# Kernel tuning notes

Hardware: AMD Instinct MI355X
Metric: run time of the kernel (lower is better)

Reference implementation:

```python
import jax, jax.numpy as jnp
import numpy as np

NUM_HEADS = 16
HEAD_DIM = 64
D_MODEL = NUM_HEADS * HEAD_DIM  # 1024
FEATURE_DIM = 2 * HEAD_DIM      # 128


def setup_inputs() -> dict:
    key = jax.random.key(0)
    ks = jax.random.split(key, 6)
    B, S = 4, 8192
    scale = D_MODEL ** -0.5
    x = jax.random.normal(ks[0], (B, S, D_MODEL), dtype=jnp.float32)
    Wq = jax.random.normal(ks[1], (D_MODEL, D_MODEL), dtype=jnp.float32) * scale
    Wk = jax.random.normal(ks[2], (D_MODEL, D_MODEL), dtype=jnp.float32) * scale
    Wv = jax.random.normal(ks[3], (D_MODEL, D_MODEL), dtype=jnp.float32) * scale
    Wo = jax.random.normal(ks[4], (D_MODEL, D_MODEL), dtype=jnp.float32) * scale
    # random_features buffer: [head_dim, feature_dim], scaled by head_dim**-0.5
    rf = jax.random.normal(ks[5], (HEAD_DIM, FEATURE_DIM), dtype=jnp.float32) * (HEAD_DIM ** -0.5)
    return {"x": x, "Wq": Wq, "Wk": Wk, "Wv": Wv, "Wo": Wo, "rf": rf}


def _phi(x, rf):
    # x: [B, H, S, head_dim] -> [B, H, S, feature_dim]
    proj = jnp.matmul(x, rf)  # [B, H, S, 2*head_dim]
    cos_p, sin_p = jnp.split(proj, 2, axis=-1)
    return jnp.concatenate([jnp.cos(cos_p), jnp.sin(sin_p)], axis=-1) * (FEATURE_DIM ** -0.5)


def reference(x, Wq, Wk, Wv, Wo, rf):
    B, S, _ = x.shape
    def heads(y):  # [B, S, D] -> [B, H, S, head_dim]
        return y.reshape(B, S, NUM_HEADS, HEAD_DIM).transpose(0, 2, 1, 3)
    Q = heads(x @ Wq)
    K = heads(x @ Wk)
    V = heads(x @ Wv)
    Qp = _phi(Q, rf)  # [B, H, S, F]
    Kp = _phi(K, rf)
    KV = jnp.einsum('bhsf,bhsd->bhfd', Kp, V)        # [B, H, F, head_dim]
    QKV = jnp.einsum('bhsf,bhfd->bhsd', Qp, KV)      # [B, H, S, head_dim]
    Z = jnp.einsum('bhsf,bhf->bhs', Qp, Kp.sum(axis=2))[..., None]
    Z = jnp.clip(Z, 1e-6, None)
    out = (QKV / Z).transpose(0, 2, 1, 3).reshape(B, S, D_MODEL)
    return out @ Wo
```

## Files before the change

### kernel.cpp

```cpp
#include <hip/hip_runtime.h>
#include <stdint.h>


#define DEVINL __device__ __forceinline__

typedef float f32x4 __attribute__((ext_vector_type(4)));
typedef __bf16 bf16x8 __attribute__((ext_vector_type(8)));
typedef unsigned short u16;

#define TSTR 136
#define RSTR 72

DEVINL u16 f2bf(float f) {
  union { float f; uint32_t u; } v; v.f = f;
  uint32_t u = v.u;
  u += 0x7fffu + ((u >> 16) & 1u);
  return (u16)(u >> 16);
}
DEVINL float bf2f(u16 h) {
  union { uint32_t u; float f; } v; v.u = ((uint32_t)h) << 16;
  return v.f;
}

#define GLOAD16(gp, lp) __builtin_amdgcn_global_load_lds( \
    (const __attribute__((address_space(1))) unsigned int*)(gp), \
    (__attribute__((address_space(3))) unsigned int*)(lp), 16, 0, 0)

template <int ROWS>
DEVINL void stage_r128(const uint8_t* g, size_t stride, u16* lds, int wave, int lane) {
#pragma unroll
  for (int j = 0; j < ROWS / 32; ++j) {
    int row = wave * (ROWS / 4) + j * 8 + (lane >> 3);
    GLOAD16(g + (size_t)row * stride + (size_t)(lane & 7) * 16,
            (uint8_t*)lds + (size_t)(wave * (ROWS / 4) + j * 8) * 128);
  }
}

template <int ROWS>
DEVINL void stage_r256(const uint8_t* g, size_t stride, u16* lds, int wave, int lane) {
#pragma unroll
  for (int j = 0; j < ROWS / 16; ++j) {
    int row = wave * (ROWS / 4) + j * 4 + (lane >> 4);
    GLOAD16(g + (size_t)row * stride + (size_t)(lane & 15) * 16,
            (uint8_t*)lds + (size_t)(wave * (ROWS / 4) + j * 4) * 256);
  }
}

DEVINL void stage128_sw(const uint8_t* g, size_t stride, u16* lds, int wave, int lane) {
  const int c = (lane & 7) ^ (lane >> 3);
#pragma unroll
  for (int j = 0; j < 4; ++j) {
    int row = wave * 32 + j * 8 + (lane >> 3);
    GLOAD16(g + (size_t)row * stride + (size_t)c * 16,
            (uint8_t*)lds + (size_t)(wave * 32 + j * 8) * 128);
  }
}

DEVINL void mma128_sw(const u16* As, const u16* Bs, f32x4 acc[4][4],
                      int wr, int wc, int lane) {
#pragma unroll
  for (int kk = 0; kk < 2; ++kk) {
    const int cw = kk * 4 + (lane >> 4);
    const int sw = (cw ^ (lane & 7)) * 8;
    bf16x8 a[4], b[4];
#pragma unroll
    for (int m = 0; m < 4; ++m)
      a[m] = *(const bf16x8*)&As[(size_t)(wr * 64 + m * 16 + (lane & 15)) * 64 + sw];
#pragma unroll
    for (int n = 0; n < 4; ++n)
      b[n] = *(const bf16x8*)&Bs[(size_t)(wc * 64 + n * 16 + (lane & 15)) * 64 + sw];
#pragma unroll
    for (int m = 0; m < 4; ++m)
#pragma unroll
      for (int n = 0; n < 4; ++n)
        acc[m][n] = __builtin_amdgcn_mfma_f32_16x16x32_bf16(a[m], b[n], acc[m][n], 0, 0, 0);
  }
}


__global__ __launch_bounds__(256) void cast_x_kernel(
    const float* __restrict__ src, u16* __restrict__ dst, long n4) {
  long i = (long)blockIdx.x * 256 + threadIdx.x;
  const long stride = (long)gridDim.x * 256;
  const float4* s4 = (const float4*)src;
  uint2* d4 = (uint2*)dst;
  for (; i < n4; i += stride) {
    float4 v = s4[i];
    uint2 o;
    o.x = (uint32_t)f2bf(v.x) | ((uint32_t)f2bf(v.y) << 16);
    o.y = (uint32_t)f2bf(v.z) | ((uint32_t)f2bf(v.w) << 16);
    d4[i] = o;
  }
}

__global__ __launch_bounds__(256) void transpose_cast_kernel(
    const float* __restrict__ src, u16* __restrict__ dst, int R, int C) {
  __shared__ float tile[32 * 33];
  const int ntr = R >> 5;
  const int tr = blockIdx.x % ntr, tc = blockIdx.x / ntr;
  const int tid = threadIdx.x;
  {
    int r = tid >> 3, c4 = (tid & 7) * 4;
    float4 v = *(const float4*)&src[(size_t)(tr * 32 + r) * C + tc * 32 + c4];
    tile[r * 33 + c4 + 0] = v.x;
    tile[r * 33 + c4 + 1] = v.y;
    tile[r * 33 + c4 + 2] = v.z;
    tile[r * 33 + c4 + 3] = v.w;
  }
  __syncthreads();
  {
    int c = tid >> 3, r4 = (tid & 7) * 4;
    uint2 o;
    o.x = (uint32_t)f2bf(tile[(r4 + 0) * 33 + c]) |
          ((uint32_t)f2bf(tile[(r4 + 1) * 33 + c]) << 16);
    o.y = (uint32_t)f2bf(tile[(r4 + 2) * 33 + c]) |
          ((uint32_t)f2bf(tile[(r4 + 3) * 33 + c]) << 16);
    *(uint2*)&dst[(size_t)(tc * 32 + c) * R + tr * 32 + r4] = o;
  }
}

__global__ __launch_bounds__(256, 3) void gemm_qkv_phi_kernel(
    const u16* __restrict__ xb, const u16* __restrict__ wT,
    const u16* __restrict__ rfT,
    u16* __restrict__ Qp, u16* __restrict__ KpT, u16* __restrict__ VhT) {
  __shared__ u16 smem[26624];
  u16* As = smem;
  u16* Bs = smem + 8192;
  u16* Rs = smem + 17408;
  const int tid = threadIdx.x, lane = tid & 63, wave = tid >> 6;
  const int wr = wave >> 1, wc = wave & 1;
  const int nb = (blockIdx.x & 7) * 768 + (blockIdx.x >> 3);
  const int tn = nb % 24, tm = nb / 24;
  const int tensor = tn >> 3;

  f32x4 acc[4][4];
#pragma unroll
  for (int m = 0; m < 4; ++m)
#pragma unroll
    for (int n = 0; n < 4; ++n) acc[m][n] = (f32x4){0.f, 0.f, 0.f, 0.f};

  const uint8_t* aB = (const uint8_t*)(xb + (size_t)tm * 128 * 1024);
  const uint8_t* bB = (const uint8_t*)(wT + (size_t)tn * 128 * 1024);
  for (int kt = 0; kt < 16; ++kt) {
    stage128_sw(aB + kt * 128, 2048, As, wave, lane);
    stage128_sw(bB + kt * 128, 2048, Bs, wave, lane);
    __syncthreads();
    mma128_sw(As, Bs, acc, wr, wc, lane);
    __syncthreads();
  }

  const int b = (tm * 128) >> 13;
  const int sblk = (tm * 128) & 8191;

  if (tensor == 2) {
#pragma unroll
    for (int m = 0; m < 4; ++m) {
      int sl = wr * 64 + m * 16 + (lane >> 4) * 4;
#pragma unroll
      for (int n = 0; n < 4; ++n) {
        int cl = wc * 64 + n * 16 + (lane & 15);
#pragma unroll
        for (int r = 0; r < 4; ++r) smem[cl * TSTR + sl + r] = f2bf(acc[m][n][r]);
      }
    }
    __syncthreads();
#pragma unroll
    for (int it = 0; it < 8; ++it) {
      int cl = it * 16 + (tid >> 4);
      int c = (tn & 7) * 128 + cl;
      int h = c >> 6, d = c & 63;
      size_t off = ((size_t)((b * 16 + h) * 64 + d)) * 8192 + sblk + (tid & 15) * 8;
      *(uint4*)&VhT[off] = *(const uint4*)&smem[cl * TSTR + (tid & 15) * 8];
    }
    return;
  }

#pragma unroll
  for (int m = 0; m < 4; ++m) {
    int sl = wr * 64 + m * 16 + (lane >> 4) * 4;
#pragma unroll
    for (int n = 0; n < 4; ++n) {
      int cl = wc * 64 + n * 16 + (lane & 15);
#pragma unroll
      for (int r = 0; r < 4; ++r) smem[(sl + r) * TSTR + cl] = f2bf(acc[m][n][r]);
    }
  }
#pragma unroll
  for (int p4 = 0; p4 < 4; ++p4) {
    int idx = p4 * 256 + tid;
    int f = idx >> 3, c = idx & 7;
    *(uint4*)&Rs[f * RSTR + c * 8] = *(const uint4*)&rfT[f * 64 + c * 8];
  }
  __syncthreads();

  bf16x8 afr[2][2][2];
#pragma unroll
  for (int hh = 0; hh < 2; ++hh)
#pragma unroll
    for (int kk = 0; kk < 2; ++kk) {
      const int ko = kk * 32 + (lane >> 4) * 8;
#pragma unroll
      for (int m = 0; m < 2; ++m)
        afr[hh][kk][m] = *(const bf16x8*)&smem[
            (size_t)(wave * 32 + m * 16 + (lane & 15)) * TSTR + hh * 64 + ko];
    }
  __syncthreads();

  const float SC = 0.088388347648318447f;
#pragma unroll
  for (int hh = 0; hh < 2; ++hh) {
    const int h = (tn & 7) * 2 + hh;
    f32x4 p[2][8];
#pragma unroll
    for (int m = 0; m < 2; ++m)
#pragma unroll
      for (int n = 0; n < 8; ++n) p[m][n] = (f32x4){0.f, 0.f, 0.f, 0.f};
#pragma unroll
    for (int kk = 0; kk < 2; ++kk) {
      const int ko = kk * 32 + (lane >> 4) * 8;
      bf16x8 bb[8];
#pragma unroll
      for (int n = 0; n < 8; ++n)
        bb[n] = *(const bf16x8*)&Rs[(size_t)(n * 16 + (lane & 15)) * RSTR + ko];
#pragma unroll
      for (int m = 0; m < 2; ++m)
#pragma unroll
        for (int n = 0; n < 8; ++n)
          p[m][n] = __builtin_amdgcn_mfma_f32_16x16x32_bf16(afr[hh][kk][m], bb[n], p[m][n], 0, 0, 0);
    }

    if (tensor == 0) {
#pragma unroll
      for (int m = 0; m < 2; ++m)
#pragma unroll
        for (int n = 0; n < 8; ++n) {
          int f = n * 16 + (lane & 15);
          int sl = wave * 32 + m * 16 + (lane >> 4) * 4;
#pragma unroll
          for (int r = 0; r < 4; ++r) {
            float v = ((n < 4) ? __cosf(p[m][n][r]) : __sinf(p[m][n][r])) * SC;
            smem[(sl + r) * TSTR + f] = f2bf(v);
          }
        }
      __syncthreads();
      const size_t base_bh = (size_t)(b * 16 + h) * 8192;
#pragma unroll
      for (int it = 0; it < 8; ++it) {
        int s = it * 16 + (tid >> 4);
        *(uint4*)&Qp[(base_bh + sblk + s) * 128 + (tid & 15) * 8] =
            *(const uint4*)&smem[s * TSTR + (tid & 15) * 8];
      }
    } else {
#pragma unroll
      for (int m = 0; m < 2; ++m)
#pragma unroll
        for (int n = 0; n < 8; ++n) {
          int f = n * 16 + (lane & 15);
          int sl = wave * 32 + m * 16 + (lane >> 4) * 4;
#pragma unroll
          for (int r = 0; r < 4; ++r) {
            float v = ((n < 4) ? __cosf(p[m][n][r]) : __sinf(p[m][n][r])) * SC;
            smem[f * TSTR + sl + r] = f2bf(v);
          }
        }
      __syncthreads();
#pragma unroll
      for (int it = 0; it < 8; ++it) {
        int f = it * 16 + (tid >> 4);
        *(uint4*)&KpT[((size_t)(b * 16 + h) * 128 + f) * 8192 + sblk + (tid & 15) * 8] =
            *(const uint4*)&smem[f * TSTR + (tid & 15) * 8];
      }
    }
    if (hh == 0) __syncthreads();
  }
}

__global__ __launch_bounds__(256) void kv_partial_kernel(
    const u16* __restrict__ KpT, const u16* __restrict__ VhT,
    float* __restrict__ partial) {
  __shared__ u16 smem[12288];
  __shared__ float ksmem[256];
  u16* As = smem;
  u16* Bs = smem + 8192;
  const int tid = threadIdx.x, lane = tid & 63, wave = tid >> 6;
  const int bh = blockIdx.x >> 3, ch = blockIdx.x & 7;
  const uint8_t* aB = (const uint8_t*)(KpT + (size_t)bh * 128 * 8192 + ch * 1024);
  const uint8_t* bB = (const uint8_t*)(VhT + (size_t)bh * 64 * 8192 + ch * 1024);

  f32x4 acc[2][4];
#pragma unroll
  for (int m = 0; m < 2; ++m)
#pragma unroll
    for (int n = 0; n < 4; ++n) acc[m][n] = (f32x4){0.f, 0.f, 0.f, 0.f};
  float ks = 0.f;
  const int fK = tid >> 1, sO = (tid & 1) * 32;

  for (int t = 0; t < 16; ++t) {
    stage_r128<128>(aB + t * 128, 16384, As, wave, lane);
    stage_r128<64>(bB + t * 128, 16384, Bs, wave, lane);
    __syncthreads();
#pragma unroll
    for (int i = 0; i < 4; ++i) {
      uint4 v = *(const uint4*)&As[fK * 64 + sO + i * 8];
      ks += bf2f((u16)(v.x & 0xffff)) + bf2f((u16)(v.x >> 16));
      ks += bf2f((u16)(v.y & 0xffff)) + bf2f((u16)(v.y >> 16));
      ks += bf2f((u16)(v.z & 0xffff)) + bf2f((u16)(v.z >> 16));
      ks += bf2f((u16)(v.w & 0xffff)) + bf2f((u16)(v.w >> 16));
    }
#pragma unroll
    for (int kk = 0; kk < 2; ++kk) {
      const int ko = kk * 32 + (lane >> 4) * 8;
      bf16x8 a[2], bb[4];
#pragma unroll
      for (int m = 0; m < 2; ++m)
        a[m] = *(const bf16x8*)&As[(size_t)(wave * 32 + m * 16 + (lane & 15)) * 64 + ko];
#pragma unroll
      for (int n = 0; n < 4; ++n)
        bb[n] = *(const bf16x8*)&Bs[(size_t)(n * 16 + (lane & 15)) * 64 + ko];
#pragma unroll
      for (int m = 0; m < 2; ++m)
#pragma unroll
        for (int n = 0; n < 4; ++n)
          acc[m][n] = __builtin_amdgcn_mfma_f32_16x16x32_bf16(a[m], bb[n], acc[m][n], 0, 0, 0);
    }
    __syncthreads();
  }

  float* pb = partial + (size_t)blockIdx.x * (128 * 65);
#pragma unroll
  for (int m = 0; m < 2; ++m)
#pragma unroll
    for (int n = 0; n < 4; ++n) {
      int d = n * 16 + (lane & 15);
#pragma unroll
      for (int r = 0; r < 4; ++r) {
        int f = wave * 32 + m * 16 + (lane >> 4) * 4 + r;
        pb[f * 65 + d] = acc[m][n][r];
      }
    }
  ksmem[tid] = ks;
  __syncthreads();
  if (tid < 128) pb[tid * 65 + 64] = ksmem[2 * tid] + ksmem[2 * tid + 1];
}

__global__ __launch_bounds__(256) void kv_reduce_kernel(
    const float* __restrict__ partial, u16* __restrict__ KVT) {
  const int bh = blockIdx.x, tid = threadIdx.x;
  for (int e = tid; e < 8320; e += 256) {
    float s = 0.f;
#pragma unroll
    for (int c = 0; c < 8; ++c) s += partial[(size_t)(bh * 8 + c) * 8320 + e];
    int f = e / 65, col = e % 65;
    KVT[((size_t)bh * 80 + col) * 128 + f] = f2bf(s);
  }
  for (int i = tid; i < 15 * 128; i += 256)
    KVT[((size_t)bh * 80 + 65) * 128 + i] = 0;
}

__global__ __launch_bounds__(256) void qkv_div_kernel(
    const u16* __restrict__ Qp, const u16* __restrict__ KVT, u16* __restrict__ A) {
  __shared__ u16 smem[26624];
  u16* Qs = smem;
  u16* Ks = smem + 16384;
  const int tid = threadIdx.x, lane = tid & 63, wave = tid >> 6;
  const int bh = blockIdx.x >> 6, st = blockIdx.x & 63;

  stage_r256<128>((const uint8_t*)(Qp + ((size_t)bh * 8192 + st * 128) * 128), 256,
                  Qs, wave, lane);
  stage_r256<80>((const uint8_t*)(KVT + (size_t)bh * 80 * 128), 256, Ks, wave, lane);
  __syncthreads();

  f32x4 acc[2][5];
#pragma unroll
  for (int m = 0; m < 2; ++m)
#pragma unroll
    for (int n = 0; n < 5; ++n) acc[m][n] = (f32x4){0.f, 0.f, 0.f, 0.f};

#pragma unroll
  for (int kk = 0; kk < 4; ++kk) {
    const int ko = kk * 32 + (lane >> 4) * 8;
    bf16x8 a[2], bb[5];
#pragma unroll
    for (int m = 0; m < 2; ++m)
      a[m] = *(const bf16x8*)&Qs[(size_t)(wave * 32 + m * 16 + (lane & 15)) * 128 + ko];
#pragma unroll
    for (int n = 0; n < 5; ++n)
      bb[n] = *(const bf16x8*)&Ks[(size_t)(n * 16 + (lane & 15)) * 128 + ko];
#pragma unroll
    for (int m = 0; m < 2; ++m)
#pragma unroll
      for (int n = 0; n < 5; ++n)
        acc[m][n] = __builtin_amdgcn_mfma_f32_16x16x32_bf16(a[m], bb[n], acc[m][n], 0, 0, 0);
  }

  const int b_ = bh >> 4, h = bh & 15;
#pragma unroll
  for (int m = 0; m < 2; ++m) {
#pragma unroll
    for (int r = 0; r < 4; ++r) {
      float z = fmaxf(__shfl(acc[m][4][r], lane & 48), 1e-6f);
      int srow = st * 128 + wave * 32 + m * 16 + (lane >> 4) * 4 + r;
      size_t rowb = ((size_t)b_ * 8192 + srow) * 1024 + h * 64;
#pragma unroll
      for (int n = 0; n < 4; ++n)
        A[rowb + n * 16 + (lane & 15)] = f2bf(acc[m][n][r] / z);
    }
  }
}

__global__ __launch_bounds__(256, 3) void gemm_out_kernel(
    const u16* __restrict__ A, const u16* __restrict__ WoT, float* __restrict__ out) {
  __shared__ u16 smem[16384];
  u16* As = smem;
  u16* Bs = smem + 8192;
  const int tid = threadIdx.x, lane = tid & 63, wave = tid >> 6;
  const int wr = wave >> 1, wc = wave & 1;
  const int nb = (blockIdx.x & 7) * 256 + (blockIdx.x >> 3);
  const int tn = nb & 7, tm = nb >> 3;

  f32x4 acc[4][4];
#pragma unroll
  for (int m = 0; m < 4; ++m)
#pragma unroll
    for (int n = 0; n < 4; ++n) acc[m][n] = (f32x4){0.f, 0.f, 0.f, 0.f};

  const uint8_t* aB = (const uint8_t*)(A + (size_t)tm * 128 * 1024);
  const uint8_t* bB = (const uint8_t*)(WoT + (size_t)tn * 128 * 1024);
  for (int kt = 0; kt < 16; ++kt) {
    stage128_sw(aB + kt * 128, 2048, As, wave, lane);
    stage128_sw(bB + kt * 128, 2048, Bs, wave, lane);
    __syncthreads();
    mma128_sw(As, Bs, acc, wr, wc, lane);
    __syncthreads();
  }

  const int rowbase = tm * 128 + wr * 64;
  const int colbase = tn * 128 + wc * 64;
#pragma unroll
  for (int m = 0; m < 4; ++m)
#pragma unroll
    for (int n = 0; n < 4; ++n) {
      int col = colbase + n * 16 + (lane & 15);
      int row = rowbase + m * 16 + (lane >> 4) * 4;
#pragma unroll
      for (int r = 0; r < 4; ++r)
        out[(size_t)(row + r) * 1024 + col] = acc[m][n][r];
    }
}


extern "C" void kernel_launch(void* const* d_in, const int* in_sizes, int n_in,
                              void* d_out, int out_size, void* d_ws, size_t ws_size,
                              hipStream_t stream) {
  const float* x  = (const float*)d_in[0];
  const float* Wq = (const float*)d_in[1];
  const float* Wk = (const float*)d_in[2];
  const float* Wv = (const float*)d_in[3];
  const float* Wo = (const float*)d_in[4];
  const float* rf = (const float*)d_in[5];
  float* out = (float*)d_out;

  if (ws_size < (size_t)411058176) return;

  u16* ws = (u16*)d_ws;
  u16* xb    = ws;
  u16* Qp    = ws + 33554432UL;
  u16* KpT   = ws + 100663296UL;
  u16* VhT   = ws + 167772160UL;
  u16* wqkvT = ws + 201326592UL;
  u16* woT   = ws + 204472320UL;
  u16* rfT   = ws + 205520896UL;
  float* partial = (float*)xb;
  u16* KVT   = wqkvT;
  u16* Abuf  = xb;

  cast_x_kernel<<<4096, 256, 0, stream>>>(x, xb, 8388608L);
  transpose_cast_kernel<<<1024, 256, 0, stream>>>(Wq, wqkvT,            1024, 1024);
  transpose_cast_kernel<<<1024, 256, 0, stream>>>(Wk, wqkvT + 1048576,  1024, 1024);
  transpose_cast_kernel<<<1024, 256, 0, stream>>>(Wv, wqkvT + 2097152,  1024, 1024);
  transpose_cast_kernel<<<1024, 256, 0, stream>>>(Wo, woT,              1024, 1024);
  transpose_cast_kernel<<<8,    256, 0, stream>>>(rf, rfT,              64,   128);

  gemm_qkv_phi_kernel<<<6144, 256, 0, stream>>>(xb, wqkvT, rfT, Qp, KpT, VhT);
  kv_partial_kernel<<<512, 256, 0, stream>>>(KpT, VhT, partial);
  kv_reduce_kernel<<<64, 256, 0, stream>>>(partial, KVT);
  qkv_div_kernel<<<4096, 256, 0, stream>>>(Qp, KVT, Abuf);
  gemm_out_kernel<<<2048, 256, 0, stream>>>(Abuf, woT, out);
}
```

Baseline: 561.7 us.

## Triple-buffer GEMM K-loop with async prefetch and split KV partials finer

After: 607.7 us. +8.2%, slower.

```diff
diff --git a/kernel.cpp b/kernel.cpp
--- a/kernel.cpp
+++ b/kernel.cpp
@@ -35,7 +35,6 @@
             (uint8_t*)lds + (size_t)(wave * (ROWS / 4) + j * 8) * 128);
   }
 }
-
 template <int ROWS>
 DEVINL void stage_r256(const uint8_t* g, size_t stride, u16* lds, int wave, int lane) {
 #pragma unroll
@@ -46,34 +45,63 @@
   }
 }
 
-DEVINL void stage128_sw(const uint8_t* g, size_t stride, u16* lds, int wave, int lane) {
-  const int c = (lane & 7) ^ (lane >> 3);
-#pragma unroll
-  for (int j = 0; j < 4; ++j) {
-    int row = wave * 32 + j * 8 + (lane >> 3);
-    GLOAD16(g + (size_t)row * stride + (size_t)c * 16,
-            (uint8_t*)lds + (size_t)(wave * 32 + j * 8) * 128);
-  }
-}
-
-DEVINL void mma128_sw(const u16* As, const u16* Bs, f32x4 acc[4][4],
-                      int wr, int wc, int lane) {
-#pragma unroll
-  for (int kk = 0; kk < 2; ++kk) {
-    const int cw = kk * 4 + (lane >> 4);
-    const int sw = (cw ^ (lane & 7)) * 8;
+DEVINL void stage_slot32(const u16* gA, const u16* gB, u16* slot, int kt, int tid) {
+  const int koff = kt * 64;
+#pragma unroll
+  for (int l = 0; l < 2; ++l) {
+    int ia = l * 256 + tid;
+    int ra = ia >> 2, sa = ia & 3;
+    int ca = (sa - (ra >> 1)) & 3;
+    GLOAD16((const uint8_t*)gA + (size_t)ra * 2048 + koff + ca * 16,
+            (uint8_t*)slot + (size_t)(ia & ~63) * 16);
+    int rb = ra, sb = sa;
+    int cb = ca;
+    GLOAD16((const uint8_t*)gB + (size_t)rb * 2048 + koff + cb * 16,
+            (uint8_t*)(slot + 4096) + (size_t)(ia & ~63) * 16);
+  }
+}
+
+DEVINL bf16x8 frd32(const u16* base, int row, int c0) {
+  int cp = (c0 + (row >> 1)) & 3;
+  return *(const bf16x8*)&base[(size_t)row * 32 + cp * 8];
+}
+
+DEVINL void gemm_main32(const u16* gA, const u16* gB, u16* smem,
+                        f32x4 acc[4][4], int tid, int lane, int wr, int wc) {
+  stage_slot32(gA, gB, smem, 0, tid);
+  stage_slot32(gA, gB, smem + 8192, 1, tid);
+  const int c0 = lane >> 4;
+  int slot_idx = 0;
+  for (int t = 0; t < 32; ++t) {
+    u16* sl = smem + slot_idx * 8192;
+    if (t < 30) {
+      int nxt = slot_idx + 2; if (nxt >= 3) nxt -= 3;
+      stage_slot32(gA, gB, smem + nxt * 8192, t + 2, tid);
+      asm volatile("s_waitcnt vmcnt(8)" ::: "memory");
+    } else if (t == 30) {
+      asm volatile("s_waitcnt vmcnt(4)" ::: "memory");
+    } else {
+      asm volatile("s_waitcnt vmcnt(0)" ::: "memory");
+    }
+    __builtin_amdgcn_s_barrier();
+    asm volatile("" ::: "memory");
     bf16x8 a[4], b[4];
 #pragma unroll
     for (int m = 0; m < 4; ++m)
-      a[m] = *(const bf16x8*)&As[(size_t)(wr * 64 + m * 16 + (lane & 15)) * 64 + sw];
+      a[m] = frd32(sl, wr * 64 + m * 16 + (lane & 15), c0);
 #pragma unroll
     for (int n = 0; n < 4; ++n)
-      b[n] = *(const bf16x8*)&Bs[(size_t)(wc * 64 + n * 16 + (lane & 15)) * 64 + sw];
+      b[n] = frd32(sl + 4096, wc * 64 + n * 16 + (lane & 15), c0);
+    __builtin_amdgcn_s_setprio(1);
 #pragma unroll
     for (int m = 0; m < 4; ++m)
 #pragma unroll
       for (int n = 0; n < 4; ++n)
         acc[m][n] = __builtin_amdgcn_mfma_f32_16x16x32_bf16(a[m], b[n], acc[m][n], 0, 0, 0);
+    __builtin_amdgcn_s_setprio(0);
+    __builtin_amdgcn_s_barrier();
+    asm volatile("" ::: "memory");
+    if (++slot_idx == 3) slot_idx = 0;
   }
 }
 
@@ -124,8 +152,6 @@
     const u16* __restrict__ rfT,
     u16* __restrict__ Qp, u16* __restrict__ KpT, u16* __restrict__ VhT) {
   __shared__ u16 smem[26624];
-  u16* As = smem;
-  u16* Bs = smem + 8192;
   u16* Rs = smem + 17408;
   const int tid = threadIdx.x, lane = tid & 63, wave = tid >> 6;
   const int wr = wave >> 1, wc = wave & 1;
@@ -139,15 +165,8 @@
 #pragma unroll
     for (int n = 0; n < 4; ++n) acc[m][n] = (f32x4){0.f, 0.f, 0.f, 0.f};
 
-  const uint8_t* aB = (const uint8_t*)(xb + (size_t)tm * 128 * 1024);
-  const uint8_t* bB = (const uint8_t*)(wT + (size_t)tn * 128 * 1024);
-  for (int kt = 0; kt < 16; ++kt) {
-    stage128_sw(aB + kt * 128, 2048, As, wave, lane);
-    stage128_sw(bB + kt * 128, 2048, Bs, wave, lane);
-    __syncthreads();
-    mma128_sw(As, Bs, acc, wr, wc, lane);
-    __syncthreads();
-  }
+  gemm_main32(xb + (size_t)tm * 128 * 1024, wT + (size_t)tn * 128 * 1024,
+              smem, acc, tid, lane, wr, wc);
 
   const int b = (tm * 128) >> 13;
   const int sblk = (tm * 128) & 8191;
@@ -278,14 +297,14 @@
 __global__ __launch_bounds__(256) void kv_partial_kernel(
     const u16* __restrict__ KpT, const u16* __restrict__ VhT,
     float* __restrict__ partial) {
-  __shared__ u16 smem[12288];
+  __shared__ u16 smem2[12288];
   __shared__ float ksmem[256];
-  u16* As = smem;
-  u16* Bs = smem + 8192;
+  u16* As = smem2;
+  u16* Bs = smem2 + 8192;
   const int tid = threadIdx.x, lane = tid & 63, wave = tid >> 6;
-  const int bh = blockIdx.x >> 3, ch = blockIdx.x & 7;
-  const uint8_t* aB = (const uint8_t*)(KpT + (size_t)bh * 128 * 8192 + ch * 1024);
-  const uint8_t* bB = (const uint8_t*)(VhT + (size_t)bh * 64 * 8192 + ch * 1024);
+  const int bh = blockIdx.x >> 4, ch = blockIdx.x & 15;
+  const uint8_t* aB = (const uint8_t*)(KpT + (size_t)bh * 128 * 8192 + ch * 512);
+  const uint8_t* bB = (const uint8_t*)(VhT + (size_t)bh * 64 * 8192 + ch * 512);
 
   f32x4 acc[2][4];
 #pragma unroll
@@ -295,7 +314,7 @@
   float ks = 0.f;
   const int fK = tid >> 1, sO = (tid & 1) * 32;
 
-  for (int t = 0; t < 16; ++t) {
+  for (int t = 0; t < 8; ++t) {
     stage_r128<128>(aB + t * 128, 16384, As, wave, lane);
     stage_r128<64>(bB + t * 128, 16384, Bs, wave, lane);
     __syncthreads();
@@ -349,7 +368,7 @@
   for (int e = tid; e < 8320; e += 256) {
     float s = 0.f;
 #pragma unroll
-    for (int c = 0; c < 8; ++c) s += partial[(size_t)(bh * 8 + c) * 8320 + e];
+    for (int c = 0; c < 16; ++c) s += partial[(size_t)(bh * 16 + c) * 8320 + e];
     int f = e / 65, col = e % 65;
     KVT[((size_t)bh * 80 + col) * 128 + f] = f2bf(s);
   }
@@ -359,9 +378,9 @@
 
 __global__ __launch_bounds__(256) void qkv_div_kernel(
     const u16* __restrict__ Qp, const u16* __restrict__ KVT, u16* __restrict__ A) {
-  __shared__ u16 smem[26624];
-  u16* Qs = smem;
-  u16* Ks = smem + 16384;
+  __shared__ u16 smem2[26624];
+  u16* Qs = smem2;
+  u16* Ks = smem2 + 16384;
   const int tid = threadIdx.x, lane = tid & 63, wave = tid >> 6;
   const int bh = blockIdx.x >> 6, st = blockIdx.x & 63;
 
@@ -410,9 +429,7 @@
 
 __global__ __launch_bounds__(256, 3) void gemm_out_kernel(
     const u16* __restrict__ A, const u16* __restrict__ WoT, float* __restrict__ out) {
-  __shared__ u16 smem[16384];
-  u16* As = smem;
-  u16* Bs = smem + 8192;
+  __shared__ u16 smem[24576];
   const int tid = threadIdx.x, lane = tid & 63, wave = tid >> 6;
   const int wr = wave >> 1, wc = wave & 1;
   const int nb = (blockIdx.x & 7) * 256 + (blockIdx.x >> 3);
@@ -424,15 +441,8 @@
 #pragma unroll
     for (int n = 0; n < 4; ++n) acc[m][n] = (f32x4){0.f, 0.f, 0.f, 0.f};
 
-  const uint8_t* aB = (const uint8_t*)(A + (size_t)tm * 128 * 1024);
-  const uint8_t* bB = (const uint8_t*)(WoT + (size_t)tn * 128 * 1024);
-  for (int kt = 0; kt < 16; ++kt) {
-    stage128_sw(aB + kt * 128, 2048, As, wave, lane);
-    stage128_sw(bB + kt * 128, 2048, Bs, wave, lane);
-    __syncthreads();
-    mma128_sw(As, Bs, acc, wr, wc, lane);
-    __syncthreads();
-  }
+  gemm_main32(A + (size_t)tm * 128 * 1024, WoT + (size_t)tn * 128 * 1024,
+              smem, acc, tid, lane, wr, wc);
 
   const int rowbase = tm * 128 + wr * 64;
   const int colbase = tn * 128 + wc * 64;
@@ -482,7 +492,7 @@
   transpose_cast_kernel<<<8,    256, 0, stream>>>(rf, rfT,              64,   128);
 
   gemm_qkv_phi_kernel<<<6144, 256, 0, stream>>>(xb, wqkvT, rfT, Qp, KpT, VhT);
-  kv_partial_kernel<<<512, 256, 0, stream>>>(KpT, VhT, partial);
+  kv_partial_kernel<<<1024, 256, 0, stream>>>(KpT, VhT, partial);
   kv_reduce_kernel<<<64, 256, 0, stream>>>(partial, KVT);
   qkv_div_kernel<<<4096, 256, 0, stream>>>(Qp, KVT, Abuf);
   gemm_out_kernel<<<2048, 256, 0, stream>>>(Abuf, woT, out);
```
